# Optimization experiments

Measured on AMD Instinct MI355X. Metric: run time of the kernel, lower is better.

The kernel has to match this reference:

```python
import jax, jax.numpy as jnp
import numpy as np
import math

B, N, D, H, FFN = 4, 2048, 512, 8, 2048
DK = D // H
EPS = 1e-5


def _layer_norm(x, g, b):
    mu = jnp.mean(x, axis=-1, keepdims=True)
    var = jnp.mean((x - mu) ** 2, axis=-1, keepdims=True)
    return (x - mu) * jax.lax.rsqrt(var + EPS) * g + b


def _rotate_half(x):
    h = x.shape[-1] // 2
    return jnp.concatenate([-x[..., h:], x[..., :h]], axis=-1)


def _rope(q, k, positions):
    # q, k: (B, H, N, DK); positions: (B, N) int
    inv_freq = 1.0 / (10000.0 ** (jnp.arange(0, DK, 2, dtype=jnp.float32) / DK))  # (DK/2,)
    ang = positions[:, None, :, None].astype(jnp.float32) * inv_freq  # (B,1,N,DK/2)
    cos = jnp.concatenate([jnp.cos(ang), jnp.cos(ang)], axis=-1)  # (B,1,N,DK)
    sin = jnp.concatenate([jnp.sin(ang), jnp.sin(ang)], axis=-1)
    q = q * cos + _rotate_half(q) * sin
    k = k * cos + _rotate_half(k) * sin
    return q, k


def setup_inputs() -> dict:
    key = jax.random.key(0)
    ks = jax.random.split(key, 16)
    s = 0.02
    x = jax.random.normal(ks[0], (B, N, D), dtype=jnp.float32)
    # backward-looking hop mask within jobs: random boolean with True diagonal
    m = jax.random.uniform(ks[1], (B, N, N)) < 0.1
    o2o_mask = m | jnp.eye(N, dtype=bool)[None]
    positions = jax.random.randint(ks[2], (B, N), 0, N)
    params = {
        'wq': jax.random.normal(ks[3], (D, D)) * s, 'bq': jnp.zeros((D,)),
        'wk': jax.random.normal(ks[4], (D, D)) * s, 'bk': jnp.zeros((D,)),
        'wv': jax.random.normal(ks[5], (D, D)) * s, 'bv': jnp.zeros((D,)),
        'wo': jax.random.normal(ks[6], (D, D)) * s, 'bo': jnp.zeros((D,)),
        'ln1_g': jnp.ones((D,)), 'ln1_b': jnp.zeros((D,)),
        'ln2_g': jnp.ones((D,)), 'ln2_b': jnp.zeros((D,)),
        'w1': jax.random.normal(ks[7], (D, FFN)) * s, 'b1': jnp.zeros((FFN,)),
        'w2': jax.random.normal(ks[8], (FFN, D)) * s, 'b2': jnp.zeros((D,)),
    }
    return {'x': x, 'o2o_mask': o2o_mask, 'positions': positions, **params}


def reference(x, o2o_mask, positions, wq, bq, wk, bk, wv, bv, wo, bo,
              ln1_g, ln1_b, ln2_g, ln2_b, w1, b1, w2, b2):
    residual = x
    xn = _layer_norm(x, ln1_g, ln1_b)
    q = (xn @ wq + bq).reshape(B, N, H, DK).transpose(0, 2, 1, 3)
    k = (xn @ wk + bk).reshape(B, N, H, DK).transpose(0, 2, 1, 3)
    v = (xn @ wv + bv).reshape(B, N, H, DK).transpose(0, 2, 1, 3)
    q, k = _rope(q, k, positions)
    scores = jnp.einsum('bhqd,bhkd->bhqk', q, k) / math.sqrt(DK)
    scores = jnp.where(o2o_mask[:, None], scores, -jnp.inf)
    attn = jax.nn.softmax(scores, axis=-1)
    attn = jnp.where(jnp.isnan(attn), 0.0, attn)  # fully-masked rows -> 0
    attn_out = jnp.einsum('bhqk,bhkd->bhqd', attn, v)
    attn_out = attn_out.transpose(0, 2, 1, 3).reshape(B, N, D)
    x = residual + (attn_out @ wo + bo)
    residual = x
    h = _layer_norm(x, ln2_g, ln2_b)
    h = jax.nn.relu(h @ w1 + b1) @ w2 + b2
    return residual + h
```

## Files before the change

### kernel.cpp

```cpp
#include <hip/hip_runtime.h>
#include <hip/hip_bf16.h>
#include <math.h>

typedef __attribute__((ext_vector_type(8))) __bf16 bf16x8;
typedef __attribute__((ext_vector_type(4))) __bf16 bf16x4;
typedef __attribute__((ext_vector_type(4))) float f32x4;

#define B_ 4
#define N_ 2048
#define D_ 512
#define H_ 8
#define DK_ 64
#define F_ 2048

__device__ __forceinline__ void async16(const __bf16* g, __bf16* l) {
  __builtin_amdgcn_global_load_lds((const __attribute__((address_space(1))) void*)g,
                                   (__attribute__((address_space(3))) void*)l, 16, 0, 0);
}

__global__ __launch_bounds__(256) void prep_all(const float* __restrict__ wq,
                                                const float* __restrict__ wk,
                                                const float* __restrict__ wv,
                                                const float* __restrict__ wo,
                                                const float* __restrict__ w1,
                                                const float* __restrict__ w2,
                                                const float* __restrict__ bq,
                                                const float* __restrict__ bk,
                                                const float* __restrict__ bv,
                                                __bf16* __restrict__ wqkvt,
                                                __bf16* __restrict__ wot,
                                                __bf16* __restrict__ w1t,
                                                __bf16* __restrict__ w2t,
                                                float* __restrict__ bqkv) {
  const int id = blockIdx.x;
  if (id >= 768) {
    int i = (id - 768) * 256 + threadIdx.x;
    bqkv[i] = (i < 512) ? bq[i] : (i < 1024) ? bk[i - 512] : bv[i - 1024];
    return;
  }
  __shared__ float t[64][65];
  const float* in;
  __bf16* outp;
  int k0, n0, K, Nc;
  if (id < 256) {
    const float* src[4] = {wq, wk, wv, wo};
    __bf16* dst[4] = {wqkvt, wqkvt + 512 * 512, wqkvt + 1024 * 512, wot};
    int w = id >> 6, tl = id & 63;
    in = src[w]; outp = dst[w]; k0 = (tl & 7) * 64; n0 = (tl >> 3) * 64; K = 512; Nc = 512;
  } else if (id < 512) {
    int tl = id - 256;
    in = w1; outp = w1t; k0 = (tl & 7) * 64; n0 = (tl >> 3) * 64; K = 512; Nc = 2048;
  } else {
    int tl = id - 512;
    in = w2; outp = w2t; k0 = (tl & 31) * 64; n0 = (tl >> 5) * 64; K = 2048; Nc = 512;
  }
  const int c = threadIdx.x & 63, r4 = threadIdx.x >> 6;
#pragma unroll
  for (int p = 0; p < 16; p++) {
    int rr = p * 4 + r4;
    t[rr][c] = in[(size_t)(k0 + rr) * Nc + n0 + c];
  }
  __syncthreads();
#pragma unroll
  for (int p = 0; p < 16; p++) {
    int rr = p * 4 + r4;
    outp[(size_t)(n0 + rr) * K + k0 + c] = (__bf16)t[c][rr];
  }
}

__global__ __launch_bounds__(256) void build_bitmask(const int* __restrict__ mask,
                                                     unsigned long long* __restrict__ bm) {
  size_t t = (size_t)blockIdx.x * 256 + threadIdx.x;
  int m = mask[t];
  unsigned long long w = __ballot(m != 0);
  if ((threadIdx.x & 63) == 0) bm[t >> 6] = w;
}

__global__ __launch_bounds__(256) void ln_fwd(const float* __restrict__ x,
                                              const float* __restrict__ g,
                                              const float* __restrict__ b,
                                              __bf16* __restrict__ out) {
  int row = blockIdx.x * 4 + (threadIdx.x >> 6);
  int lane = threadIdx.x & 63;
  const float* xr = x + (size_t)row * D_ + lane * 8;
  float4 a0 = *(const float4*)xr;
  float4 a1 = *(const float4*)(xr + 4);
  float v[8] = {a0.x, a0.y, a0.z, a0.w, a1.x, a1.y, a1.z, a1.w};
  float s = 0.f;
#pragma unroll
  for (int i = 0; i < 8; i++) s += v[i];
#pragma unroll
  for (int off = 1; off < 64; off <<= 1) s += __shfl_xor(s, off);
  float mu = s * (1.f / D_);
  float q = 0.f;
#pragma unroll
  for (int i = 0; i < 8; i++) { float d = v[i] - mu; q += d * d; }
#pragma unroll
  for (int off = 1; off < 64; off <<= 1) q += __shfl_xor(q, off);
  float rs = rsqrtf(q * (1.f / D_) + 1e-5f);
  const float* gp = g + lane * 8;
  const float* bp = b + lane * 8;
  alignas(16) __bf16 o[8];
#pragma unroll
  for (int i = 0; i < 8; i++) o[i] = (__bf16)((v[i] - mu) * rs * gp[i] + bp[i]);
  *(bf16x8*)(out + (size_t)row * D_ + lane * 8) = *(bf16x8*)o;
}

__global__ __launch_bounds__(256) void rope_vtrans(const __bf16* __restrict__ qkv,
                                                   const int* __restrict__ pos,
                                                   __bf16* __restrict__ qo,
                                                   __bf16* __restrict__ ko,
                                                   __bf16* __restrict__ vt) {
  __shared__ __bf16 tl[64][65];
  const int id = blockIdx.x;
  if (id < 8192) {
    int t = id * 256 + threadIdx.x;
    int d = t & 31;
    int h = (t >> 5) & 7;
    int n = (t >> 8) & (N_ - 1);
    int b = t >> 19;
    const __bf16* base = qkv + (size_t)(b * N_ + n) * 1536 + h * 64 + d;
    float q1 = (float)base[0], q2 = (float)base[32];
    float k1 = (float)base[512], k2 = (float)base[544];
    float p = (float)pos[b * N_ + n];
    float inv = __expf(-(float)d * (9.210340371976184f / 32.f));
    float ang = p * inv;
    float sn, cs;
    sincosf(ang, &sn, &cs);
    size_t ob = ((size_t)(b * H_ + h) * N_ + n) * DK_ + d;
    qo[ob]      = (__bf16)(q1 * cs - q2 * sn);
    qo[ob + 32] = (__bf16)(q2 * cs + q1 * sn);
    ko[ob]      = (__bf16)(k1 * cs - k2 * sn);
    ko[ob + 32] = (__bf16)(k2 * cs + k1 * sn);
  } else {
    const int lin = id - 8192;
    const int n0 = (lin & 31) * 64, h = (lin >> 5) & 7, b = lin >> 8;
    const int c = threadIdx.x & 63, rr = threadIdx.x >> 6;
#pragma unroll
    for (int p = 0; p < 16; p++) {
      int i = p * 4 + rr;
      tl[i][c] = qkv[(size_t)(b * N_ + n0 + i) * 1536 + 1024 + h * 64 + c];
    }
    __syncthreads();
    size_t ob = (size_t)(b * H_ + h) * DK_ * N_;
#pragma unroll
    for (int p = 0; p < 16; p++) {
      int dd = p * 4 + rr;
      vt[ob + (size_t)dd * N_ + n0 + c] = tl[c][dd];
    }
  }
}

template <int RELU, int OBF, int RES>
__global__ __launch_bounds__(256) void gemm_bt(const __bf16* __restrict__ A,
                                               const __bf16* __restrict__ Bt,
                                               const float* __restrict__ bias,
                                               const float* __restrict__ res,
                                               void* __restrict__ Cout,
                                               int M, int N, int K) {
  __shared__ __bf16 As[2][128 * 32];
  __shared__ __bf16 Bs[2][128 * 32];
  const int tid = threadIdx.x;
  const int lane = tid & 63;
  const int wave = tid >> 6;
  const int quad = lane >> 4;
  const int l16 = lane & 15;
  const int m0 = blockIdx.y * 128;
  const int n0 = blockIdx.x * 128;
  const int wm = (wave >> 1) * 64;
  const int wn = (wave & 1) * 64;
  f32x4 acc[4][4] = {};

  const int c0 = tid, c1 = tid + 256;
  const int ar0 = c0 >> 2, ak0 = (c0 & 3) * 8;
  const int ar1 = c1 >> 2, ak1 = (c1 & 3) * 8;

  auto stage = [&](int k0, int buf) {
    async16(A + (size_t)(m0 + ar0) * K + k0 + ak0, As[buf] + c0 * 8);
    async16(A + (size_t)(m0 + ar1) * K + k0 + ak1, As[buf] + c1 * 8);
    async16(Bt + (size_t)(n0 + ar0) * K + k0 + ak0, Bs[buf] + c0 * 8);
    async16(Bt + (size_t)(n0 + ar1) * K + k0 + ak1, Bs[buf] + c1 * 8);
  };

  stage(0, 0);
  __syncthreads();
  const int niter = K >> 5;
  for (int it = 0; it < niter; it++) {
    const int buf = it & 1;
    if (it + 1 < niter) stage((it + 1) * 32, buf ^ 1);
    bf16x8 af[4], bf[4];
#pragma unroll
    for (int mi = 0; mi < 4; mi++)
      af[mi] = *(const bf16x8*)(As[buf] + (wm + mi * 16 + l16) * 32 + quad * 8);
#pragma unroll
    for (int ni = 0; ni < 4; ni++)
      bf[ni] = *(const bf16x8*)(Bs[buf] + (wn + ni * 16 + l16) * 32 + quad * 8);
#pragma unroll
    for (int mi = 0; mi < 4; mi++)
#pragma unroll
      for (int ni = 0; ni < 4; ni++)
        acc[mi][ni] = __builtin_amdgcn_mfma_f32_16x16x32_bf16(af[mi], bf[ni], acc[mi][ni], 0, 0, 0);
    __syncthreads();
  }
#pragma unroll
  for (int ni = 0; ni < 4; ni++) {
    const int col = n0 + wn + ni * 16 + l16;
    const float bv = bias[col];
#pragma unroll
    for (int mi = 0; mi < 4; mi++) {
#pragma unroll
      for (int r = 0; r < 4; r++) {
        const int row = m0 + wm + mi * 16 + quad * 4 + r;
        float v = acc[mi][ni][r] + bv;
        if (RES) v += res[(size_t)row * N + col];
        if (RELU) v = fmaxf(v, 0.f);
        if (OBF) ((__bf16*)Cout)[(size_t)row * N + col] = (__bf16)v;
        else     ((float*)Cout)[(size_t)row * N + col] = v;
      }
    }
  }
}

template <int RELU, int OBF, int RES>
__global__ __launch_bounds__(256) void gemm_bt64(const __bf16* __restrict__ A,
                                                 const __bf16* __restrict__ Bt,
                                                 const float* __restrict__ bias,
                                                 const float* __restrict__ res,
                                                 void* __restrict__ Cout,
                                                 int M, int N, int K) {
  __shared__ __bf16 As[2][128 * 32];
  __shared__ __bf16 Bs[2][64 * 32];
  const int tid = threadIdx.x;
  const int lane = tid & 63;
  const int wave = tid >> 6;
  const int quad = lane >> 4;
  const int l16 = lane & 15;
  const int m0 = blockIdx.y * 128;
  const int n0 = blockIdx.x * 64;
  const int wm = wave * 32;
  f32x4 acc[2][4] = {};

  const int ar0 = tid >> 2, ak0 = (tid & 3) * 8;

  auto stage = [&](int k0, int buf) {
    async16(A + (size_t)(m0 + ar0) * K + k0 + ak0, As[buf] + tid * 8);
    async16(A + (size_t)(m0 + 64 + ar0) * K + k0 + ak0, As[buf] + (tid + 256) * 8);
    async16(Bt + (size_t)(n0 + ar0) * K + k0 + ak0, Bs[buf] + tid * 8);
  };

  stage(0, 0);
  __syncthreads();
  const int niter = K >> 5;
  for (int it = 0; it < niter; it++) {
    const int buf = it & 1;
    if (it + 1 < niter) stage((it + 1) * 32, buf ^ 1);
    bf16x8 af[2], bf[4];
#pragma unroll
    for (int mi = 0; mi < 2; mi++)
      af[mi] = *(const bf16x8*)(As[buf] + (wm + mi * 16 + l16) * 32 + quad * 8);
#pragma unroll
    for (int ni = 0; ni < 4; ni++)
      bf[ni] = *(const bf16x8*)(Bs[buf] + (ni * 16 + l16) * 32 + quad * 8);
#pragma unroll
    for (int mi = 0; mi < 2; mi++)
#pragma unroll
      for (int ni = 0; ni < 4; ni++)
        acc[mi][ni] = __builtin_amdgcn_mfma_f32_16x16x32_bf16(af[mi], bf[ni], acc[mi][ni], 0, 0, 0);
    __syncthreads();
  }
#pragma unroll
  for (int ni = 0; ni < 4; ni++) {
    const int col = n0 + ni * 16 + l16;
    const float bv = bias[col];
#pragma unroll
    for (int mi = 0; mi < 2; mi++) {
#pragma unroll
      for (int r = 0; r < 4; r++) {
        const int row = m0 + wm + mi * 16 + quad * 4 + r;
        float v = acc[mi][ni][r] + bv;
        if (RES) v += res[(size_t)row * N + col];
        if (RELU) v = fmaxf(v, 0.f);
        if (OBF) ((__bf16*)Cout)[(size_t)row * N + col] = (__bf16)v;
        else     ((float*)Cout)[(size_t)row * N + col] = v;
      }
    }
  }
}

__global__ __launch_bounds__(256, 2) void flash_attn(const __bf16* __restrict__ q,
                                                     const __bf16* __restrict__ k,
                                                     const __bf16* __restrict__ vt,
                                                     const unsigned long long* __restrict__ bm,
                                                     __bf16* __restrict__ out) {
  const int qt = blockIdx.x, h = blockIdx.y, b = blockIdx.z;
  const int tid = threadIdx.x;
  const int lane = tid & 63, wave = tid >> 6;
  const int quad = lane >> 4, l16 = lane & 15;
  __shared__ __bf16 Ks[2][64 * 64];
  __shared__ __bf16 Vs[2][64 * 64];
  __shared__ __bf16 P[4][2][16 * 68];
  const size_t bh = (size_t)b * H_ + h;
  const __bf16* qp = q + (bh * N_ + qt * 128 + wave * 32) * DK_;
  bf16x8 qf[2][2];
#pragma unroll
  for (int s = 0; s < 2; s++)
#pragma unroll
    for (int ks = 0; ks < 2; ks++) {
      qf[s][ks] = *(const bf16x8*)(qp + (s * 16 + l16) * DK_ + ks * 32 + quad * 8);
#pragma unroll
      for (int j = 0; j < 8; j++) qf[s][ks][j] = qf[s][ks][j] * (__bf16)0.125f;
    }
  const __bf16* kbase = k + bh * N_ * DK_;
  const __bf16* vbase = vt + bh * DK_ * N_;
  const int qrow0 = qt * 128 + wave * 32 + l16;
  const unsigned long long* bmr0 = bm + (size_t)(b * N_ + qrow0) * (N_ / 64);
  const unsigned long long* bmr1 = bmr0 + 16 * (N_ / 64);
  const int xo = l16 & 7;

  f32x4 oacc[2][4] = {};
  float lsum[2] = {0.f, 0.f};

  auto stage = [&](int kt, int buf) {
    const __bf16* kg = kbase + (size_t)kt * 64 * DK_;
    const __bf16* vg = vbase + kt * 64;
#pragma unroll
    for (int i = 0; i < 2; i++) {
      const int s = tid + i * 256;
      const int r = s >> 3;
      const int j = (s & 7) ^ (r & 7);
      async16(kg + r * DK_ + j * 8, Ks[buf] + s * 8);
      async16(vg + (size_t)r * N_ + j * 8, Vs[buf] + s * 8);
    }
  };

  stage(0, 0);
  __syncthreads();

  for (int kt = 0; kt < N_ / 64; kt++) {
    const int buf = kt & 1;
    if (kt + 1 < N_ / 64) stage(kt + 1, buf ^ 1);

    const unsigned long long mw0 = bmr0[kt] >> (quad * 4);
    const unsigned long long mw1 = bmr1[kt] >> (quad * 4);
#pragma unroll
    for (int ci = 0; ci < 4; ci++) {
      const int row = ci * 16 + l16;
      bf16x8 kf0 = *(const bf16x8*)(Ks[buf] + (row * 8 + (quad ^ xo)) * 8);
      bf16x8 kf1 = *(const bf16x8*)(Ks[buf] + (row * 8 + ((4 + quad) ^ xo)) * 8);
#pragma unroll
      for (int s = 0; s < 2; s++) {
        f32x4 a = {0.f, 0.f, 0.f, 0.f};
        a = __builtin_amdgcn_mfma_f32_16x16x32_bf16(kf0, qf[s][0], a, 0, 0, 0);
        a = __builtin_amdgcn_mfma_f32_16x16x32_bf16(kf1, qf[s][1], a, 0, 0, 0);
        const unsigned long long mw = s ? mw1 : mw0;
        bf16x4 pk;
#pragma unroll
        for (int r = 0; r < 4; r++) {
          float in = ((mw >> (ci * 16 + r)) & 1ull) ? a[r] : -1e30f;
          float p = __expf(in);
          lsum[s] += p;
          pk[r] = (__bf16)p;
        }
        *(bf16x4*)(&P[wave][s][0] + l16 * 68 + ci * 16 + quad * 4) = pk;
      }
    }
    bf16x8 pf[2][2];
#pragma unroll
    for (int s = 0; s < 2; s++) {
      pf[s][0] = *(const bf16x8*)(&P[wave][s][0] + l16 * 68 + quad * 8);
      pf[s][1] = *(const bf16x8*)(&P[wave][s][0] + l16 * 68 + 32 + quad * 8);
    }
#pragma unroll
    for (int ni = 0; ni < 4; ni++) {
      const int row = ni * 16 + l16;
      bf16x8 vf0 = *(const bf16x8*)(Vs[buf] + (row * 8 + (quad ^ xo)) * 8);
      bf16x8 vf1 = *(const bf16x8*)(Vs[buf] + (row * 8 + ((4 + quad) ^ xo)) * 8);
#pragma unroll
      for (int s = 0; s < 2; s++) {
        oacc[s][ni] = __builtin_amdgcn_mfma_f32_16x16x32_bf16(vf0, pf[s][0], oacc[s][ni], 0, 0, 0);
        oacc[s][ni] = __builtin_amdgcn_mfma_f32_16x16x32_bf16(vf1, pf[s][1], oacc[s][ni], 0, 0, 0);
      }
    }
    __syncthreads();
  }
#pragma unroll
  for (int s = 0; s < 2; s++) {
    lsum[s] += __shfl_xor(lsum[s], 16);
    lsum[s] += __shfl_xor(lsum[s], 32);
    const float inv_l = (lsum[s] > 0.f) ? 1.f / lsum[s] : 0.f;
#pragma unroll
    for (int ni = 0; ni < 4; ni++) {
      bf16x4 ov;
#pragma unroll
      for (int r = 0; r < 4; r++) ov[r] = (__bf16)(oacc[s][ni][r] * inv_l);
      *(bf16x4*)(out + ((size_t)b * N_ + qrow0 + s * 16) * D_ + h * DK_ + ni * 16 + quad * 4) = ov;
    }
  }
}

static constexpr size_t OFF_XN  = 0;
static constexpr size_t OFF_WT  = 8388608;
static constexpr size_t OFF_WO  = OFF_WT + 1572864;
static constexpr size_t OFF_W1  = OFF_WO + 524288;
static constexpr size_t OFF_W2  = OFF_W1 + 2097152;
static constexpr size_t OFF_BQ  = OFF_W2 + 2097152;
static constexpr size_t OFF_QKV = OFF_BQ + 6144;
static constexpr size_t OFF_QR  = OFF_QKV + 25165824;
static constexpr size_t OFF_KR  = OFF_QR + 8388608;
static constexpr size_t OFF_VT  = OFF_KR + 8388608;
static constexpr size_t OFF_AO  = OFF_VT + 8388608;
static constexpr size_t OFF_Y   = OFF_AO + 8388608;

extern "C" void kernel_launch(void* const* d_in, const int* in_sizes, int n_in,
                              void* d_out, int out_size, void* d_ws, size_t ws_size,
                              hipStream_t stream) {
  const float* x    = (const float*)d_in[0];
  const int*   mask = (const int*)d_in[1];
  const int*   pos  = (const int*)d_in[2];
  const float* wq   = (const float*)d_in[3];
  const float* bq   = (const float*)d_in[4];
  const float* wk   = (const float*)d_in[5];
  const float* bk   = (const float*)d_in[6];
  const float* wv   = (const float*)d_in[7];
  const float* bv   = (const float*)d_in[8];
  const float* wo   = (const float*)d_in[9];
  const float* bo   = (const float*)d_in[10];
  const float* ln1g = (const float*)d_in[11];
  const float* ln1b = (const float*)d_in[12];
  const float* ln2g = (const float*)d_in[13];
  const float* ln2b = (const float*)d_in[14];
  const float* w1   = (const float*)d_in[15];
  const float* b1   = (const float*)d_in[16];
  const float* w2   = (const float*)d_in[17];
  const float* b2   = (const float*)d_in[18];
  float* out = (float*)d_out;
  char* ws = (char*)d_ws;

  __bf16* xn    = (__bf16*)(ws + OFF_XN);
  __bf16* wqkvt = (__bf16*)(ws + OFF_WT);
  __bf16* wot   = (__bf16*)(ws + OFF_WO);
  __bf16* w1t   = (__bf16*)(ws + OFF_W1);
  __bf16* w2t   = (__bf16*)(ws + OFF_W2);
  float*  bqkv  = (float*)(ws + OFF_BQ);
  __bf16* qkv   = (__bf16*)(ws + OFF_QKV);
  __bf16* qr    = (__bf16*)(ws + OFF_QR);
  __bf16* kr    = (__bf16*)(ws + OFF_KR);
  __bf16* vt    = (__bf16*)(ws + OFF_VT);
  __bf16* attn  = (__bf16*)(ws + OFF_AO);
  float*  y     = (float*)(ws + OFF_Y);
  unsigned long long* bm = (unsigned long long*)(ws + OFF_Y);
  __bf16* hn    = xn;
  __bf16* h2    = qkv;

  dim3 b256(256);
  prep_all<<<774, b256, 0, stream>>>(wq, wk, wv, wo, w1, w2, bq, bk, bv,
                                     wqkvt, wot, w1t, w2t, bqkv);
  build_bitmask<<<65536, b256, 0, stream>>>(mask, bm);
  ln_fwd<<<2048, b256, 0, stream>>>(x, ln1g, ln1b, xn);
  gemm_bt<0, 1, 0><<<dim3(12, 64), b256, 0, stream>>>(xn, wqkvt, bqkv, nullptr, qkv, 8192, 1536, 512);
  rope_vtrans<<<9216, b256, 0, stream>>>(qkv, pos, qr, kr, vt);
  flash_attn<<<dim3(16, 8, 4), b256, 0, stream>>>(qr, kr, vt, bm, attn);
  gemm_bt64<0, 0, 1><<<dim3(8, 64), b256, 0, stream>>>(attn, wot, bo, x, y, 8192, 512, 512);
  ln_fwd<<<2048, b256, 0, stream>>>(y, ln2g, ln2b, hn);
  gemm_bt<1, 1, 0><<<dim3(16, 64), b256, 0, stream>>>(hn, w1t, b1, nullptr, h2, 8192, 2048, 512);
  gemm_bt64<0, 0, 1><<<dim3(8, 64), b256, 0, stream>>>(h2, w2t, b2, y, out, 8192, 512, 2048);
}
```

Measured before the change: 377.4 us.

## Split attention work across 8 waves of 16 query rows each

```diff
diff --git a/kernel.cpp b/kernel.cpp
--- a/kernel.cpp
+++ b/kernel.cpp
@@ -287,7 +287,7 @@
   }
 }
 
-__global__ __launch_bounds__(256, 2) void flash_attn(const __bf16* __restrict__ q,
+__global__ __launch_bounds__(512, 4) void flash_attn(const __bf16* __restrict__ q,
                                                      const __bf16* __restrict__ k,
                                                      const __bf16* __restrict__ vt,
                                                      const unsigned long long* __restrict__ bm,
@@ -298,39 +298,33 @@
   const int quad = lane >> 4, l16 = lane & 15;
   __shared__ __bf16 Ks[2][64 * 64];
   __shared__ __bf16 Vs[2][64 * 64];
-  __shared__ __bf16 P[4][2][16 * 68];
+  __shared__ __bf16 P[8][16 * 68];
   const size_t bh = (size_t)b * H_ + h;
-  const __bf16* qp = q + (bh * N_ + qt * 128 + wave * 32) * DK_;
-  bf16x8 qf[2][2];
-#pragma unroll
-  for (int s = 0; s < 2; s++)
-#pragma unroll
-    for (int ks = 0; ks < 2; ks++) {
-      qf[s][ks] = *(const bf16x8*)(qp + (s * 16 + l16) * DK_ + ks * 32 + quad * 8);
-#pragma unroll
-      for (int j = 0; j < 8; j++) qf[s][ks][j] = qf[s][ks][j] * (__bf16)0.125f;
-    }
+  const __bf16* qp = q + (bh * N_ + qt * 128 + wave * 16) * DK_;
+  bf16x8 qf[2];
+#pragma unroll
+  for (int ks = 0; ks < 2; ks++) {
+    qf[ks] = *(const bf16x8*)(qp + l16 * DK_ + ks * 32 + quad * 8);
+#pragma unroll
+    for (int j = 0; j < 8; j++) qf[ks][j] = qf[ks][j] * (__bf16)0.125f;
+  }
   const __bf16* kbase = k + bh * N_ * DK_;
   const __bf16* vbase = vt + bh * DK_ * N_;
-  const int qrow0 = qt * 128 + wave * 32 + l16;
-  const unsigned long long* bmr0 = bm + (size_t)(b * N_ + qrow0) * (N_ / 64);
-  const unsigned long long* bmr1 = bmr0 + 16 * (N_ / 64);
+  const int qrow0 = qt * 128 + wave * 16 + l16;
+  const unsigned long long* bmr = bm + (size_t)(b * N_ + qrow0) * (N_ / 64);
   const int xo = l16 & 7;
 
-  f32x4 oacc[2][4] = {};
-  float lsum[2] = {0.f, 0.f};
+  f32x4 oacc[4] = {};
+  float lsum = 0.f;
 
   auto stage = [&](int kt, int buf) {
     const __bf16* kg = kbase + (size_t)kt * 64 * DK_;
     const __bf16* vg = vbase + kt * 64;
-#pragma unroll
-    for (int i = 0; i < 2; i++) {
-      const int s = tid + i * 256;
-      const int r = s >> 3;
-      const int j = (s & 7) ^ (r & 7);
-      async16(kg + r * DK_ + j * 8, Ks[buf] + s * 8);
-      async16(vg + (size_t)r * N_ + j * 8, Vs[buf] + s * 8);
-    }
+    const int s = tid;
+    const int r = s >> 3;
+    const int j = (s & 7) ^ (r & 7);
+    async16(kg + r * DK_ + j * 8, Ks[buf] + s * 8);
+    async16(vg + (size_t)r * N_ + j * 8, Vs[buf] + s * 8);
   };
 
   stage(0, 0);
@@ -340,61 +334,47 @@
     const int buf = kt & 1;
     if (kt + 1 < N_ / 64) stage(kt + 1, buf ^ 1);
 
-    const unsigned long long mw0 = bmr0[kt] >> (quad * 4);
-    const unsigned long long mw1 = bmr1[kt] >> (quad * 4);
+    const unsigned long long mw = bmr[kt] >> (quad * 4);
 #pragma unroll
     for (int ci = 0; ci < 4; ci++) {
       const int row = ci * 16 + l16;
       bf16x8 kf0 = *(const bf16x8*)(Ks[buf] + (row * 8 + (quad ^ xo)) * 8);
       bf16x8 kf1 = *(const bf16x8*)(Ks[buf] + (row * 8 + ((4 + quad) ^ xo)) * 8);
-#pragma unroll
-      for (int s = 0; s < 2; s++) {
-        f32x4 a = {0.f, 0.f, 0.f, 0.f};
-        a = __builtin_amdgcn_mfma_f32_16x16x32_bf16(kf0, qf[s][0], a, 0, 0, 0);
-        a = __builtin_amdgcn_mfma_f32_16x16x32_bf16(kf1, qf[s][1], a, 0, 0, 0);
-        const unsigned long long mw = s ? mw1 : mw0;
-        bf16x4 pk;
-#pragma unroll
-        for (int r = 0; r < 4; r++) {
-          float in = ((mw >> (ci * 16 + r)) & 1ull) ? a[r] : -1e30f;
-          float p = __expf(in);
-          lsum[s] += p;
-          pk[r] = (__bf16)p;
-        }
-        *(bf16x4*)(&P[wave][s][0] + l16 * 68 + ci * 16 + quad * 4) = pk;
+      f32x4 a = {0.f, 0.f, 0.f, 0.f};
+      a = __builtin_amdgcn_mfma_f32_16x16x32_bf16(kf0, qf[0], a, 0, 0, 0);
+      a = __builtin_amdgcn_mfma_f32_16x16x32_bf16(kf1, qf[1], a, 0, 0, 0);
+      const unsigned int nib = (unsigned int)(mw >> (ci * 16)) & 15u;
+      bf16x4 pk;
+#pragma unroll
+      for (int r4 = 0; r4 < 4; r4++) {
+        float in = ((nib >> r4) & 1u) ? a[r4] : -1e30f;
+        float p = __expf(in);
+        lsum += p;
+        pk[r4] = (__bf16)p;
       }
-    }
-    bf16x8 pf[2][2];
-#pragma unroll
-    for (int s = 0; s < 2; s++) {
-      pf[s][0] = *(const bf16x8*)(&P[wave][s][0] + l16 * 68 + quad * 8);
-      pf[s][1] = *(const bf16x8*)(&P[wave][s][0] + l16 * 68 + 32 + quad * 8);
-    }
+      *(bf16x4*)(&P[wave][0] + l16 * 68 + ci * 16 + quad * 4) = pk;
+    }
+    bf16x8 pf0 = *(const bf16x8*)(&P[wave][0] + l16 * 68 + quad * 8);
+    bf16x8 pf1 = *(const bf16x8*)(&P[wave][0] + l16 * 68 + 32 + quad * 8);
 #pragma unroll
     for (int ni = 0; ni < 4; ni++) {
       const int row = ni * 16 + l16;
       bf16x8 vf0 = *(const bf16x8*)(Vs[buf] + (row * 8 + (quad ^ xo)) * 8);
       bf16x8 vf1 = *(const bf16x8*)(Vs[buf] + (row * 8 + ((4 + quad) ^ xo)) * 8);
-#pragma unroll
-      for (int s = 0; s < 2; s++) {
-        oacc[s][ni] = __builtin_amdgcn_mfma_f32_16x16x32_bf16(vf0, pf[s][0], oacc[s][ni], 0, 0, 0);
-        oacc[s][ni] = __builtin_amdgcn_mfma_f32_16x16x32_bf16(vf1, pf[s][1], oacc[s][ni], 0, 0, 0);
-      }
+      oacc[ni] = __builtin_amdgcn_mfma_f32_16x16x32_bf16(vf0, pf0, oacc[ni], 0, 0, 0);
+      oacc[ni] = __builtin_amdgcn_mfma_f32_16x16x32_bf16(vf1, pf1, oacc[ni], 0, 0, 0);
     }
     __syncthreads();
   }
-#pragma unroll
-  for (int s = 0; s < 2; s++) {
-    lsum[s] += __shfl_xor(lsum[s], 16);
-    lsum[s] += __shfl_xor(lsum[s], 32);
-    const float inv_l = (lsum[s] > 0.f) ? 1.f / lsum[s] : 0.f;
-#pragma unroll
-    for (int ni = 0; ni < 4; ni++) {
-      bf16x4 ov;
-#pragma unroll
-      for (int r = 0; r < 4; r++) ov[r] = (__bf16)(oacc[s][ni][r] * inv_l);
-      *(bf16x4*)(out + ((size_t)b * N_ + qrow0 + s * 16) * D_ + h * DK_ + ni * 16 + quad * 4) = ov;
-    }
+  lsum += __shfl_xor(lsum, 16);
+  lsum += __shfl_xor(lsum, 32);
+  const float inv_l = (lsum > 0.f) ? 1.f / lsum : 0.f;
+#pragma unroll
+  for (int ni = 0; ni < 4; ni++) {
+    bf16x4 ov;
+#pragma unroll
+    for (int r = 0; r < 4; r++) ov[r] = (__bf16)(oacc[ni][r] * inv_l);
+    *(bf16x4*)(out + ((size_t)b * N_ + qrow0) * D_ + h * DK_ + ni * 16 + quad * 4) = ov;
   }
 }
 
@@ -453,13 +433,14 @@
   __bf16* h2    = qkv;
 
   dim3 b256(256);
+  dim3 b512(512);
   prep_all<<<774, b256, 0, stream>>>(wq, wk, wv, wo, w1, w2, bq, bk, bv,
                                      wqkvt, wot, w1t, w2t, bqkv);
   build_bitmask<<<65536, b256, 0, stream>>>(mask, bm);
   ln_fwd<<<2048, b256, 0, stream>>>(x, ln1g, ln1b, xn);
   gemm_bt<0, 1, 0><<<dim3(12, 64), b256, 0, stream>>>(xn, wqkvt, bqkv, nullptr, qkv, 8192, 1536, 512);
   rope_vtrans<<<9216, b256, 0, stream>>>(qkv, pos, qr, kr, vt);
-  flash_attn<<<dim3(16, 8, 4), b256, 0, stream>>>(qr, kr, vt, bm, attn);
+  flash_attn<<<dim3(16, 8, 4), b512, 0, stream>>>(qr, kr, vt, bm, attn);
   gemm_bt64<0, 0, 1><<<dim3(8, 64), b256, 0, stream>>>(attn, wot, bo, x, y, 8192, 512, 512);
   ln_fwd<<<2048, b256, 0, stream>>>(y, ln2g, ln2b, hn);
   gemm_bt<1, 1, 0><<<dim3(16, 64), b256, 0, stream>>>(hn, w1t, b1, nullptr, h2, 8192, 2048, 512);
```

Result: faster. 368.7 us (-2.3%).

## Split attention keys across two wave groups per block and merge partial sums

Applied to the files above, without the earlier changes.

```diff
diff --git a/kernel.cpp b/kernel.cpp
--- a/kernel.cpp
+++ b/kernel.cpp
@@ -287,7 +287,7 @@
   }
 }
 
-__global__ __launch_bounds__(256, 2) void flash_attn(const __bf16* __restrict__ q,
+__global__ __launch_bounds__(512, 4) void flash_attn(const __bf16* __restrict__ q,
                                                      const __bf16* __restrict__ k,
                                                      const __bf16* __restrict__ vt,
                                                      const unsigned long long* __restrict__ bm,
@@ -296,11 +296,14 @@
   const int tid = threadIdx.x;
   const int lane = tid & 63, wave = tid >> 6;
   const int quad = lane >> 4, l16 = lane & 15;
-  __shared__ __bf16 Ks[2][64 * 64];
-  __shared__ __bf16 Vs[2][64 * 64];
-  __shared__ __bf16 P[4][2][16 * 68];
+  const int g = wave >> 2;
+  const int wl = wave & 3;
+  __shared__ alignas(16) __bf16 smem[25600];
+  __bf16* Pw0 = smem + 16384 + wave * 1152 + l16 * 36;
+  __bf16* Pw1 = Pw0 + 576;
+
   const size_t bh = (size_t)b * H_ + h;
-  const __bf16* qp = q + (bh * N_ + qt * 128 + wave * 32) * DK_;
+  const __bf16* qp = q + (bh * N_ + qt * 128 + wl * 32) * DK_;
   bf16x8 qf[2][2];
 #pragma unroll
   for (int s = 0; s < 2; s++)
@@ -310,90 +313,124 @@
 #pragma unroll
       for (int j = 0; j < 8; j++) qf[s][ks][j] = qf[s][ks][j] * (__bf16)0.125f;
     }
-  const __bf16* kbase = k + bh * N_ * DK_;
-  const __bf16* vbase = vt + bh * DK_ * N_;
-  const int qrow0 = qt * 128 + wave * 32 + l16;
-  const unsigned long long* bmr0 = bm + (size_t)(b * N_ + qrow0) * (N_ / 64);
-  const unsigned long long* bmr1 = bmr0 + 16 * (N_ / 64);
+  const __bf16* kbase = k + bh * N_ * DK_ + (size_t)g * 1024 * DK_;
+  const __bf16* vbase = vt + bh * DK_ * N_ + g * 1024;
+  const int qrow0 = qt * 128 + wl * 32 + l16;
+  const unsigned int* bm32 = (const unsigned int*)bm;
+  const unsigned int* bmr0 = bm32 + ((size_t)(b * N_ + qrow0) * 64 + g * 32);
+  const unsigned int* bmr1 = bmr0 + 16 * 64;
   const int xo = l16 & 7;
+
+  int offK0[2], offK1[2], offV[4];
+#pragma unroll
+  for (int ci = 0; ci < 2; ci++) {
+    const int row = ci * 16 + l16;
+    offK0[ci] = (row * 8 + (quad ^ xo)) * 8;
+    offK1[ci] = (row * 8 + ((4 + quad) ^ xo)) * 8;
+  }
+#pragma unroll
+  for (int ni = 0; ni < 4; ni++) {
+    const int rowv = ni * 16 + l16;
+    offV[ni] = (rowv * 4 + (quad ^ (l16 & 3))) * 8;
+  }
 
   f32x4 oacc[2][4] = {};
   float lsum[2] = {0.f, 0.f};
 
+  const int tg = tid & 255;
+  const int rK = tg >> 3, jK = (tg & 7) ^ (rK & 7);
+  const int rV = tg >> 2, jV = (tg & 3) ^ (rV & 3);
+  const __bf16* ksrc = kbase + (size_t)rK * DK_ + jK * 8;
+  const __bf16* vsrc = vbase + (size_t)rV * N_ + jV * 8;
+
   auto stage = [&](int kt, int buf) {
-    const __bf16* kg = kbase + (size_t)kt * 64 * DK_;
-    const __bf16* vg = vbase + kt * 64;
-#pragma unroll
-    for (int i = 0; i < 2; i++) {
-      const int s = tid + i * 256;
-      const int r = s >> 3;
-      const int j = (s & 7) ^ (r & 7);
-      async16(kg + r * DK_ + j * 8, Ks[buf] + s * 8);
-      async16(vg + (size_t)r * N_ + j * 8, Vs[buf] + s * 8);
-    }
+    __bf16* KT = smem + (g * 2 + buf) * 4096;
+    async16(ksrc + (size_t)kt * (32 * DK_), KT + tg * 8);
+    async16(vsrc + kt * 32, KT + 2048 + tg * 8);
   };
 
   stage(0, 0);
+  unsigned int mw0 = bmr0[0], mw1 = bmr1[0];
   __syncthreads();
 
-  for (int kt = 0; kt < N_ / 64; kt++) {
+  for (int kt = 0; kt < 32; kt++) {
     const int buf = kt & 1;
-    if (kt + 1 < N_ / 64) stage(kt + 1, buf ^ 1);
-
-    const unsigned long long mw0 = bmr0[kt] >> (quad * 4);
-    const unsigned long long mw1 = bmr1[kt] >> (quad * 4);
-#pragma unroll
-    for (int ci = 0; ci < 4; ci++) {
-      const int row = ci * 16 + l16;
-      bf16x8 kf0 = *(const bf16x8*)(Ks[buf] + (row * 8 + (quad ^ xo)) * 8);
-      bf16x8 kf1 = *(const bf16x8*)(Ks[buf] + (row * 8 + ((4 + quad) ^ xo)) * 8);
+    if (kt + 1 < 32) stage(kt + 1, buf ^ 1);
+    unsigned int mn0 = 0, mn1 = 0;
+    if (kt + 1 < 32) { mn0 = bmr0[kt + 1]; mn1 = bmr1[kt + 1]; }
+
+    const __bf16* KT = smem + (g * 2 + buf) * 4096;
+    const __bf16* VT = KT + 2048;
+#pragma unroll
+    for (int ci = 0; ci < 2; ci++) {
+      bf16x8 kf0 = *(const bf16x8*)(KT + offK0[ci]);
+      bf16x8 kf1 = *(const bf16x8*)(KT + offK1[ci]);
 #pragma unroll
       for (int s = 0; s < 2; s++) {
         f32x4 a = {0.f, 0.f, 0.f, 0.f};
         a = __builtin_amdgcn_mfma_f32_16x16x32_bf16(kf0, qf[s][0], a, 0, 0, 0);
         a = __builtin_amdgcn_mfma_f32_16x16x32_bf16(kf1, qf[s][1], a, 0, 0, 0);
-        const unsigned long long mw = s ? mw1 : mw0;
+        const unsigned int mw = s ? mw1 : mw0;
+        const unsigned int nib = (mw >> (ci * 16 + quad * 4)) & 15u;
         bf16x4 pk;
 #pragma unroll
         for (int r = 0; r < 4; r++) {
-          float in = ((mw >> (ci * 16 + r)) & 1ull) ? a[r] : -1e30f;
+          float in = ((nib >> r) & 1u) ? a[r] : -1e30f;
           float p = __expf(in);
           lsum[s] += p;
           pk[r] = (__bf16)p;
         }
-        *(bf16x4*)(&P[wave][s][0] + l16 * 68 + ci * 16 + quad * 4) = pk;
+        *(bf16x4*)((s ? Pw1 : Pw0) + ci * 16 + quad * 4) = pk;
       }
     }
-    bf16x8 pf[2][2];
-#pragma unroll
-    for (int s = 0; s < 2; s++) {
-      pf[s][0] = *(const bf16x8*)(&P[wave][s][0] + l16 * 68 + quad * 8);
-      pf[s][1] = *(const bf16x8*)(&P[wave][s][0] + l16 * 68 + 32 + quad * 8);
-    }
+    bf16x8 pf0 = *(const bf16x8*)(Pw0 + quad * 8);
+    bf16x8 pf1 = *(const bf16x8*)(Pw1 + quad * 8);
 #pragma unroll
     for (int ni = 0; ni < 4; ni++) {
-      const int row = ni * 16 + l16;
-      bf16x8 vf0 = *(const bf16x8*)(Vs[buf] + (row * 8 + (quad ^ xo)) * 8);
-      bf16x8 vf1 = *(const bf16x8*)(Vs[buf] + (row * 8 + ((4 + quad) ^ xo)) * 8);
-#pragma unroll
-      for (int s = 0; s < 2; s++) {
-        oacc[s][ni] = __builtin_amdgcn_mfma_f32_16x16x32_bf16(vf0, pf[s][0], oacc[s][ni], 0, 0, 0);
-        oacc[s][ni] = __builtin_amdgcn_mfma_f32_16x16x32_bf16(vf1, pf[s][1], oacc[s][ni], 0, 0, 0);
-      }
-    }
+      bf16x8 vf = *(const bf16x8*)(VT + offV[ni]);
+      oacc[0][ni] = __builtin_amdgcn_mfma_f32_16x16x32_bf16(vf, pf0, oacc[0][ni], 0, 0, 0);
+      oacc[1][ni] = __builtin_amdgcn_mfma_f32_16x16x32_bf16(vf, pf1, oacc[1][ni], 0, 0, 0);
+    }
+    mw0 = mn0; mw1 = mn1;
     __syncthreads();
   }
+
 #pragma unroll
   for (int s = 0; s < 2; s++) {
     lsum[s] += __shfl_xor(lsum[s], 16);
     lsum[s] += __shfl_xor(lsum[s], 32);
-    const float inv_l = (lsum[s] > 0.f) ? 1.f / lsum[s] : 0.f;
-#pragma unroll
-    for (int ni = 0; ni < 4; ni++) {
-      bf16x4 ov;
-#pragma unroll
-      for (int r = 0; r < 4; r++) ov[r] = (__bf16)(oacc[s][ni][r] * inv_l);
-      *(bf16x4*)(out + ((size_t)b * N_ + qrow0 + s * 16) * D_ + h * DK_ + ni * 16 + quad * 4) = ov;
+  }
+
+  float* cs = (float*)smem;
+  if (wave >= 4) {
+    const int base = ((wave & 3) * 64 + lane) * 36;
+#pragma unroll
+    for (int s = 0; s < 2; s++)
+#pragma unroll
+      for (int ni = 0; ni < 4; ni++)
+        *(f32x4*)(cs + base + (s * 4 + ni) * 4) = oacc[s][ni];
+    cs[base + 32] = lsum[0];
+    cs[base + 33] = lsum[1];
+  }
+  __syncthreads();
+  if (wave < 4) {
+    const int base = (wave * 64 + lane) * 36;
+#pragma unroll
+    for (int s = 0; s < 2; s++) {
+#pragma unroll
+      for (int ni = 0; ni < 4; ni++) {
+        f32x4 o2 = *(const f32x4*)(cs + base + (s * 4 + ni) * 4);
+        oacc[s][ni] += o2;
+      }
+      const float lt = lsum[s] + cs[base + 32 + s];
+      const float inv_l = (lt > 0.f) ? 1.f / lt : 0.f;
+#pragma unroll
+      for (int ni = 0; ni < 4; ni++) {
+        bf16x4 ov;
+#pragma unroll
+        for (int r = 0; r < 4; r++) ov[r] = (__bf16)(oacc[s][ni][r] * inv_l);
+        *(bf16x4*)(out + ((size_t)b * N_ + qrow0 + s * 16) * D_ + h * DK_ + ni * 16 + quad * 4) = ov;
+      }
     }
   }
 }
@@ -453,13 +490,14 @@
   __bf16* h2    = qkv;
 
   dim3 b256(256);
+  dim3 b512(512);
   prep_all<<<774, b256, 0, stream>>>(wq, wk, wv, wo, w1, w2, bq, bk, bv,
                                      wqkvt, wot, w1t, w2t, bqkv);
   build_bitmask<<<65536, b256, 0, stream>>>(mask, bm);
   ln_fwd<<<2048, b256, 0, stream>>>(x, ln1g, ln1b, xn);
   gemm_bt<0, 1, 0><<<dim3(12, 64), b256, 0, stream>>>(xn, wqkvt, bqkv, nullptr, qkv, 8192, 1536, 512);
   rope_vtrans<<<9216, b256, 0, stream>>>(qkv, pos, qr, kr, vt);
-  flash_attn<<<dim3(16, 8, 4), b256, 0, stream>>>(qr, kr, vt, bm, attn);
+  flash_attn<<<dim3(16, 8, 4), b512, 0, stream>>>(qr, kr, vt, bm, attn);
   gemm_bt64<0, 0, 1><<<dim3(8, 64), b256, 0, stream>>>(attn, wot, bo, x, y, 8192, 512, 512);
   ln_fwd<<<2048, b256, 0, stream>>>(y, ln2g, ln2b, hn);
   gemm_bt<1, 1, 0><<<dim3(16, 64), b256, 0, stream>>>(hn, w1t, b1, nullptr, h2, 8192, 2048, 512);
```

Result: no change. 380.8 us (+0.9%).
